# Performance work log

Hardware: AMD Instinct MI355X
Metric: run time of the kernel (lower is better)

## Reference

```python
import jax, jax.numpy as jnp
import numpy as np

N, E, F, C, H, O, ED = 100000, 1600000, 64, 64, 1, 32, 16
M = 20000  # number of masked (selected) nodes


def gat_layer(x, src, dst, edge_attr, W, a_s, a_d, We, a_e, b, n, h, c):
    # x: [n, in], W: [in, h*c], a_*: [h, c], We: [ed, h*c], b: [h*c]
    hx = (x @ W).reshape(n, h, c)                       # node features per head
    alpha_s = (hx * a_s).sum(-1)                        # [n, h]
    alpha_d = (hx * a_d).sum(-1)                        # [n, h]
    he = (edge_attr @ We).reshape(-1, h, c)             # [e, h, c]
    alpha = alpha_s[src] + alpha_d[dst] + (he * a_e).sum(-1)  # [e, h]
    alpha = jax.nn.leaky_relu(alpha, 0.2)
    # segment softmax over incoming edges of each destination node
    mx = jax.ops.segment_max(alpha, dst, num_segments=n)
    ex = jnp.exp(alpha - mx[dst])
    denom = jax.ops.segment_sum(ex, dst, num_segments=n)
    coef = ex / denom[dst]                              # [e, h]
    out = jax.ops.segment_sum(coef[:, :, None] * hx[src], dst, num_segments=n)
    return out.reshape(n, h * c) + b


def setup_inputs() -> dict:
    key = jax.random.key(0)
    ks = jax.random.split(key, 16)
    s = 0.1
    inp = {
        "x": jax.random.normal(ks[0], (N, F), jnp.float32),
        "edge_index": jax.random.randint(ks[1], (2, E), 0, N, jnp.int32),
        "mask": jax.random.randint(ks[2], (M,), 0, N, jnp.int32),
        "edge_attr": jax.random.normal(ks[3], (E, ED), jnp.float32),
        # conv1 params
        "W1": jax.random.normal(ks[4], (F, H * C), jnp.float32) * s,
        "a_s1": jax.random.normal(ks[5], (H, C), jnp.float32) * s,
        "a_d1": jax.random.normal(ks[6], (H, C), jnp.float32) * s,
        "We1": jax.random.normal(ks[7], (ED, H * C), jnp.float32) * s,
        "a_e1": jax.random.normal(ks[8], (H, C), jnp.float32) * s,
        "b1": jnp.zeros((H * C,), jnp.float32),
        # conv2 params
        "W2": jax.random.normal(ks[9], (H * C, H * O), jnp.float32) * s,
        "a_s2": jax.random.normal(ks[10], (H, O), jnp.float32) * s,
        "a_d2": jax.random.normal(ks[11], (H, O), jnp.float32) * s,
        "We2": jax.random.normal(ks[12], (ED, H * O), jnp.float32) * s,
        "a_e2": jax.random.normal(ks[13], (H, O), jnp.float32) * s,
        "b2": jnp.zeros((H * O,), jnp.float32),
    }
    return inp


def reference(x, edge_index, mask, edge_attr,
              W1, a_s1, a_d1, We1, a_e1, b1,
              W2, a_s2, a_d2, We2, a_e2, b2):
    # add self loops with fill_value=0 edge attributes (GATConv fill_value=0)
    loops = jnp.arange(N, dtype=edge_index.dtype)
    src = jnp.concatenate([edge_index[0], loops])
    dst = jnp.concatenate([edge_index[1], loops])
    ea = jnp.concatenate([edge_attr, jnp.zeros((N, ED), edge_attr.dtype)], axis=0)

    h1 = jax.nn.elu(gat_layer(x, src, dst, ea, W1, a_s1, a_d1, We1, a_e1, b1, N, H, C))
    h2 = jax.nn.elu(gat_layer(h1, src, dst, ea, W2, a_s2, a_d2, We2, a_e2, b2, N, H, O))
    return h2[mask]  # [M, O]; squeeze() is a no-op here
```

## Files before the change

### kernel.cpp

```cpp
#include <hip/hip_runtime.h>
#include <hip/hip_bf16.h>
#include <hip/hip_fp16.h>
#include <math.h>

#define NN 100000
#define EE 1600000
#define MM 20000
#define EPB 768
#define NBLK ((EE + EPB - 1) / EPB)
#define NBC 250
#define BWC 400
#define N_SCAN (NBC * NBLK + 1)
#define SMASK 0x1FFFF

__global__ void k_v(const float* __restrict__ We1, const float* __restrict__ ae1v,
                    const float* __restrict__ We2, const float* __restrict__ ae2v,
                    float* __restrict__ v1, float* __restrict__ v2) {
    int t = threadIdx.x;
    if (t < 16) {
        float s = 0.f;
        for (int c = 0; c < 64; ++c) s += We1[t * 64 + c] * ae1v[c];
        v1[t] = s;
    } else if (t < 32) {
        int r = t - 16;
        float s = 0.f;
        for (int c = 0; c < 32; ++c) s += We2[r * 32 + c] * ae2v[c];
        v2[r] = s;
    }
}

__global__ __launch_bounds__(256) void k_node1(
    const float* __restrict__ x, const float* __restrict__ W,
    const float* __restrict__ a_s, const float* __restrict__ a_d,
    __half* __restrict__ hx, float* __restrict__ aS, float* __restrict__ aD,
    int n_nodes)
{
    __shared__ float Wl[64 * 64];
    __shared__ float xs[4][64];
    int tid = threadIdx.x;
#pragma unroll
    for (int i = 0; i < 16; ++i) Wl[tid + i * 256] = W[tid + i * 256];
    int wv = tid >> 6, lane = tid & 63;
    int n = blockIdx.x * 4 + wv;
    bool act = (n < n_nodes);
    if (act) xs[wv][lane] = x[(size_t)n * 64 + lane];
    __syncthreads();
    if (!act) return;
    float h = 0.f;
#pragma unroll
    for (int k = 0; k < 64; ++k) h += xs[wv][k] * Wl[k * 64 + lane];
    hx[(size_t)n * 64 + lane] = __float2half(h);
    float ps = h * a_s[lane];
    float pd = h * a_d[lane];
#pragma unroll
    for (int o = 32; o > 0; o >>= 1) { ps += __shfl_xor(ps, o); pd += __shfl_xor(pd, o); }
    if (lane == 0) { aS[n] = ps; aD[n] = pd; }
}

__global__ __launch_bounds__(256) void k_bh(const int* __restrict__ dst,
                                            int* __restrict__ bh, int E) {
    __shared__ int hl[NBC];
    int tid = threadIdx.x, blk = blockIdx.x;
    for (int j = tid; j < NBC; j += 256) hl[j] = 0;
    __syncthreads();
    int e0 = blk * EPB, e1 = min(E, e0 + EPB);
    for (int e = e0 + tid; e < e1; e += 256) atomicAdd(&hl[dst[e] / BWC], 1);
    __syncthreads();
    for (int j = tid; j < NBC; j += 256) bh[j * NBLK + blk] = hl[j];
    if (blk == 0 && tid == 0) bh[NBC * NBLK] = 0;
}

__global__ __launch_bounds__(256) void k_scan1(const int* __restrict__ deg, int* __restrict__ pre,
                                               int* __restrict__ bsum, int n) {
    __shared__ int wsum[4];
    int t = threadIdx.x;
    int base = blockIdx.x * 2048 + t * 8;
    int v[8]; int s = 0;
#pragma unroll
    for (int i = 0; i < 8; ++i) { int idx = base + i; int d = (idx < n) ? deg[idx] : 0; v[i] = s; s += d; }
    int lane = t & 63, wv = t >> 6;
    int incl = s;
#pragma unroll
    for (int off = 1; off < 64; off <<= 1) { int y = __shfl_up(incl, off); if (lane >= off) incl += y; }
    if (lane == 63) wsum[wv] = incl;
    __syncthreads();
    int woff = 0;
    for (int w = 0; w < wv; ++w) woff += wsum[w];
    int texcl = woff + incl - s;
#pragma unroll
    for (int i = 0; i < 8; ++i) { int idx = base + i; if (idx < n) pre[idx] = texcl + v[i]; }
    if (t == 255) bsum[blockIdx.x] = woff + incl;
}

__global__ __launch_bounds__(256) void k_scan2(int* __restrict__ bsum, int nb) {
    __shared__ int ws[4];
    int t = threadIdx.x, lane = t & 63, wv = t >> 6;
    int x = (t < nb) ? bsum[t] : 0;
    int incl = x;
#pragma unroll
    for (int off = 1; off < 64; off <<= 1) { int y = __shfl_up(incl, off); if (lane >= off) incl += y; }
    if (lane == 63) ws[wv] = incl;
    __syncthreads();
    int woff = 0;
    for (int w = 0; w < wv; ++w) woff += ws[w];
    if (t < nb) bsum[t] = woff + incl - x;
}

__global__ void k_scan3b(int* __restrict__ pre, const int* __restrict__ bsum, int n) {
    int i = blockIdx.x * 256 + threadIdx.x;
    if (i < n) pre[i] += bsum[i >> 11];
}

__global__ __launch_bounds__(256) void k_part(
    const float* __restrict__ ea, const float* __restrict__ v1, const float* __restrict__ v2,
    const int* __restrict__ src, const int* __restrict__ dst,
    const float* __restrict__ aS1, const float* __restrict__ aD1,
    const int* __restrict__ scanned, uint2* __restrict__ recMid, int E)
{
    __shared__ int lcur[NBC];
    int tid = threadIdx.x, blk = blockIdx.x;
    for (int j = tid; j < NBC; j += 256) lcur[j] = scanned[j * NBLK + blk];
    __syncthreads();
    const float4* v14 = (const float4*)v1;
    const float4* v24 = (const float4*)v2;
    float4 va0 = v14[0], va1 = v14[1], va2 = v14[2], va3 = v14[3];
    float4 vb0 = v24[0], vb1 = v24[1], vb2 = v24[2], vb3 = v24[3];
    int e0 = blk * EPB, e1 = min(E, e0 + EPB);
    for (int e = e0 + tid; e < e1; e += 256) {
        const float4* p4 = (const float4*)(ea + (size_t)e * 16);
        float4 q0 = p4[0], q1 = p4[1], q2 = p4[2], q3 = p4[3];
        float s1 = q0.x * va0.x + q0.y * va0.y + q0.z * va0.z + q0.w * va0.w
                 + q1.x * va1.x + q1.y * va1.y + q1.z * va1.z + q1.w * va1.w
                 + q2.x * va2.x + q2.y * va2.y + q2.z * va2.z + q2.w * va2.w
                 + q3.x * va3.x + q3.y * va3.y + q3.z * va3.z + q3.w * va3.w;
        float s2 = q0.x * vb0.x + q0.y * vb0.y + q0.z * vb0.z + q0.w * vb0.w
                 + q1.x * vb1.x + q1.y * vb1.y + q1.z * vb1.z + q1.w * vb1.w
                 + q2.x * vb2.x + q2.y * vb2.y + q2.z * vb2.z + q2.w * vb2.w
                 + q3.x * vb3.x + q3.y * vb3.y + q3.z * vb3.z + q3.w * vb3.w;
        int s = src[e], d = dst[e];
        float a = aS1[s] + aD1[d] + s1;
        a = a > 0.f ? a : 0.2f * a;
        float ex = __expf(a);
        int b = d / BWC;
        int dloc = d - b * BWC;
        unsigned lo = (unsigned)s | ((unsigned)dloc << 17);
        unsigned hi = (unsigned)__half_as_ushort(__float2half(ex))
                    | ((unsigned)__half_as_ushort(__float2half(s2)) << 16);
        int pos = atomicAdd(&lcur[b], 1);
        recMid[pos] = make_uint2(lo, hi);
    }
}

__global__ __launch_bounds__(256) void k_build(
    const int* __restrict__ scanned, const uint2* __restrict__ recMid,
    int* __restrict__ rowptr, uint2* __restrict__ rec, int E)
{
    __shared__ int hist[BWC];
    __shared__ int lofs[BWC];
    __shared__ int wsum[4];
    int tid = threadIdx.x, b = blockIdx.x;
    int B0 = scanned[b * NBLK];
    int B1 = scanned[(b + 1) * NBLK];
    for (int j = tid; j < BWC; j += 256) hist[j] = 0;
    __syncthreads();
    for (int i = B0 + tid; i < B1; i += 256) atomicAdd(&hist[recMid[i].x >> 17], 1);
    __syncthreads();
    int lane = tid & 63, wv = tid >> 6;
    int i0 = 2 * tid, i1 = 2 * tid + 1;
    int a0 = (i0 < BWC) ? hist[i0] : 0;
    int a1 = (i1 < BWC) ? hist[i1] : 0;
    int s = a0 + a1;
    int incl = s;
#pragma unroll
    for (int off = 1; off < 64; off <<= 1) { int y = __shfl_up(incl, off); if (lane >= off) incl += y; }
    if (lane == 63) wsum[wv] = incl;
    __syncthreads();
    int woff = 0;
    for (int w = 0; w < wv; ++w) woff += wsum[w];
    int base = woff + incl - s;
    if (i0 < BWC) lofs[i0] = base;
    if (i1 < BWC) lofs[i1] = base + a0;
    __syncthreads();
    for (int j = tid; j < BWC; j += 256) rowptr[b * BWC + j] = B0 + lofs[j];
    if (b == NBC - 1 && tid == 0) rowptr[NN] = E;
    __syncthreads();
    for (int i = B0 + tid; i < B1; i += 256) {
        uint2 r = recMid[i];
        int nl = (int)(r.x >> 17);
        int p = atomicAdd(&lofs[nl], 1);
        rec[B0 + p] = r;
    }
}

__global__ __launch_bounds__(256) void k_agg1(
    const int* __restrict__ rowptr,
    const uint2* __restrict__ rec, const __half* __restrict__ hx,
    const float* __restrict__ aS, const float* __restrict__ aD,
    const float* __restrict__ b, float* __restrict__ h1, int n_nodes)
{
    int wv = threadIdx.x >> 6, lane = threadIdx.x & 63;
    int n = blockIdx.x * 4 + wv;
    if (n >= n_nodes) return;
    int start = rowptr[n], end = rowptr[n + 1];
    float r = 0.f, den = 0.f;
    for (int base = start; base < end; base += 64) {
        int cnt = min(end - base, 64);
        int s = 0; float ex = 0.f;
        if (lane < cnt) {
            uint2 R = rec[base + lane];
            s = (int)(R.x & SMASK);
            ex = __half2float(__ushort_as_half((unsigned short)(R.y & 0xFFFFu)));
        }
        int j = 0;
        for (; j + 4 <= cnt; j += 4) {
            int s0 = __shfl(s, j), s1 = __shfl(s, j + 1), s2 = __shfl(s, j + 2), s3 = __shfl(s, j + 3);
            float e0 = __shfl(ex, j), e1 = __shfl(ex, j + 1), e2 = __shfl(ex, j + 2), e3 = __shfl(ex, j + 3);
            float h0 = __half2float(hx[(size_t)s0 * 64 + lane]);
            float h1v = __half2float(hx[(size_t)s1 * 64 + lane]);
            float h2 = __half2float(hx[(size_t)s2 * 64 + lane]);
            float h3 = __half2float(hx[(size_t)s3 * 64 + lane]);
            r += e0 * h0; r += e1 * h1v; r += e2 * h2; r += e3 * h3;
            den += e0 + e1 + e2 + e3;
        }
        for (; j < cnt; ++j) {
            int sj = __shfl(s, j); float ej = __shfl(ex, j);
            r += ej * __half2float(hx[(size_t)sj * 64 + lane]);
            den += ej;
        }
    }
    float al = aS[n] + aD[n];
    al = al > 0.f ? al : 0.2f * al;
    float exl = __expf(al);
    float hself = __half2float(hx[(size_t)n * 64 + lane]);
    float val = (r + exl * hself) / (den + exl) + b[lane];
    h1[(size_t)n * 64 + lane] = val > 0.f ? val : expm1f(val);
}

__global__ __launch_bounds__(256) void k_node2(
    const float* __restrict__ h1, const float* __restrict__ W,
    const float* __restrict__ a_s, const float* __restrict__ a_d,
    float* __restrict__ hx, float* __restrict__ aS, float* __restrict__ aD, int n_nodes)
{
    __shared__ float Wl[64 * 32];
    __shared__ float xs[8][64];
    int tid = threadIdx.x;
#pragma unroll
    for (int i = 0; i < 8; ++i) Wl[tid + i * 256] = W[tid + i * 256];
    int n0 = blockIdx.x * 8;
    for (int i = tid; i < 8 * 64; i += 256) {
        int r = i >> 6;
        int n = n0 + r;
        xs[r][i & 63] = (n < n_nodes) ? h1[(size_t)n * 64 + (i & 63)] : 0.f;
    }
    __syncthreads();
    int g = tid >> 5, c = tid & 31;
    int n = n0 + g;
    if (n >= n_nodes) return;
    float h = 0.f;
#pragma unroll
    for (int k = 0; k < 64; ++k) h += xs[g][k] * Wl[k * 32 + c];
    hx[(size_t)n * 32 + c] = h;
    float ps = h * a_s[c], pd = h * a_d[c];
#pragma unroll
    for (int o = 16; o > 0; o >>= 1) { ps += __shfl_xor(ps, o, 32); pd += __shfl_xor(pd, o, 32); }
    if (c == 0) { aS[n] = ps; aD[n] = pd; }
}

__global__ __launch_bounds__(256) void k_agg2(
    const int* __restrict__ mask, const int* __restrict__ rowptr,
    const uint2* __restrict__ rec, const float* __restrict__ hx,
    const float* __restrict__ aS, const float* __restrict__ aD,
    const float* __restrict__ b, float* __restrict__ out, int m_cnt)
{
    int wv = threadIdx.x >> 6, lane = threadIdx.x & 63;
    int m = blockIdx.x * 4 + wv;
    if (m >= m_cnt) return;
    int n = mask[m];
    int start = rowptr[n], end = rowptr[n + 1];
    float aDn = aD[n];
    int half = lane >> 5, c = lane & 31;
    float r = 0.f, den = 0.f;
    for (int base = start; base < end; base += 64) {
        int cnt = min(end - base, 64);
        int s = 0; float ex = 0.f;
        if (lane < cnt) {
            uint2 R = rec[base + lane];
            s = (int)(R.x & SMASK);
            float ae2 = __half2float(__ushort_as_half((unsigned short)(R.y >> 16)));
            float a = aS[s] + aDn + ae2;
            a = a > 0.f ? a : 0.2f * a;
            ex = __expf(a);
        }
        int j = 0;
        for (; j + 8 <= cnt; j += 8) {
            int j0 = j + half, j2 = j + 2 + half, j4 = j + 4 + half, j6 = j + 6 + half;
            int s0 = __shfl(s, j0), s2v = __shfl(s, j2), s4 = __shfl(s, j4), s6 = __shfl(s, j6);
            float e0 = __shfl(ex, j0), e2 = __shfl(ex, j2), e4 = __shfl(ex, j4), e6 = __shfl(ex, j6);
            r += e0 * hx[(size_t)s0 * 32 + c];
            r += e2 * hx[(size_t)s2v * 32 + c];
            r += e4 * hx[(size_t)s4 * 32 + c];
            r += e6 * hx[(size_t)s6 * 32 + c];
            den += e0 + e2 + e4 + e6;
        }
        for (; j < cnt; j += 2) {
            int jj = j + half;
            if (jj < cnt) {
                int sj = __shfl(s, jj); float ej = __shfl(ex, jj);
                r += ej * hx[(size_t)sj * 32 + c];
                den += ej;
            }
        }
    }
    float ro = __shfl(r, lane ^ 32);
    float do_ = __shfl(den, lane ^ 32);
    r += ro; den += do_;
    if (half == 0) {
        float al = aS[n] + aDn;
        al = al > 0.f ? al : 0.2f * al;
        float exl = __expf(al);
        float val = (r + exl * hx[(size_t)n * 32 + c]) / (den + exl) + b[c];
        out[(size_t)m * 32 + c] = val > 0.f ? val : expm1f(val);
    }
}

extern "C" void kernel_launch(void* const* d_in, const int* in_sizes, int n_in,
                              void* d_out, int out_size, void* d_ws, size_t ws_size,
                              hipStream_t stream) {
    const float* x    = (const float*)d_in[0];
    const int*   ei   = (const int*)d_in[1];
    const int*   mask = (const int*)d_in[2];
    const float* ea   = (const float*)d_in[3];
    const float* W1   = (const float*)d_in[4];
    const float* a_s1 = (const float*)d_in[5];
    const float* a_d1 = (const float*)d_in[6];
    const float* We1  = (const float*)d_in[7];
    const float* a_e1 = (const float*)d_in[8];
    const float* b1   = (const float*)d_in[9];
    const float* W2   = (const float*)d_in[10];
    const float* a_s2 = (const float*)d_in[11];
    const float* a_d2 = (const float*)d_in[12];
    const float* We2  = (const float*)d_in[13];
    const float* a_e2 = (const float*)d_in[14];
    const float* b2   = (const float*)d_in[15];
    const int* src = ei;
    const int* dst = ei + EE;
    float* out = (float*)d_out;

    char* w = (char*)d_ws;
    size_t off = 0;
    auto take = [&](size_t bytes) -> char* {
        char* p = w + off;
        off += (bytes + 255) & ~(size_t)255;
        return p;
    };
    float*  v1      = (float*)take(16 * 4);
    float*  v2      = (float*)take(16 * 4);
    __half* hx1h    = (__half*)take((size_t)NN * 64 * 2);
    float*  aS1     = (float*)take((size_t)NN * 4);
    float*  aD1     = (float*)take((size_t)NN * 4);
    float*  h1      = (float*)take((size_t)NN * 64 * 4);
    float*  hx2     = (float*)take((size_t)NN * 32 * 4);
    float*  aS2     = (float*)take((size_t)NN * 4);
    float*  aD2     = (float*)take((size_t)NN * 4);
    int*    rowptr  = (int*)take(((size_t)NN + 1) * 4);
    int*    bh      = (int*)take((size_t)N_SCAN * 4);
    int*    scanned = (int*)take((size_t)N_SCAN * 4);
    int*    bsum    = (int*)take(256 * 4);
    uint2*  recMid  = (uint2*)take((size_t)EE * 8);
    uint2*  rec     = (uint2*)take((size_t)EE * 8);

    const int nb_bh = (N_SCAN + 2047) / 2048;

    k_v<<<1, 64, 0, stream>>>(We1, a_e1, We2, a_e2, v1, v2);
    k_node1<<<(NN + 3) / 4, 256, 0, stream>>>(x, W1, a_s1, a_d1, hx1h, aS1, aD1, NN);
    k_bh<<<NBLK, 256, 0, stream>>>(dst, bh, EE);
    k_scan1<<<nb_bh, 256, 0, stream>>>(bh, scanned, bsum, N_SCAN);
    k_scan2<<<1, 256, 0, stream>>>(bsum, nb_bh);
    k_scan3b<<<(N_SCAN + 255) / 256, 256, 0, stream>>>(scanned, bsum, N_SCAN);
    k_part<<<NBLK, 256, 0, stream>>>(ea, v1, v2, src, dst, aS1, aD1, scanned, recMid, EE);
    k_build<<<NBC, 256, 0, stream>>>(scanned, recMid, rowptr, rec, EE);
    k_agg1<<<(NN + 3) / 4, 256, 0, stream>>>(rowptr, rec, hx1h, aS1, aD1, b1, h1, NN);
    k_node2<<<(NN + 7) / 8, 256, 0, stream>>>(h1, W2, a_s2, a_d2, hx2, aS2, aD2, NN);
    k_agg2<<<(MM + 3) / 4, 256, 0, stream>>>(mask, rowptr, rec, hx2, aS2, aD2, b2, out, MM);
}
```

Before: 239.8 us.

## Move edge-attr projection into histogram pass and defer layer-1 exp to aggregation

```diff
diff --git a/kernel.cpp b/kernel.cpp
--- a/kernel.cpp
+++ b/kernel.cpp
@@ -57,69 +57,14 @@
     if (lane == 0) { aS[n] = ps; aD[n] = pd; }
 }
 
-__global__ __launch_bounds__(256) void k_bh(const int* __restrict__ dst,
-                                            int* __restrict__ bh, int E) {
+__global__ __launch_bounds__(256) void k_aebh(
+    const float* __restrict__ ea, const float* __restrict__ v1, const float* __restrict__ v2,
+    const int* __restrict__ dst, unsigned* __restrict__ ae12,
+    int* __restrict__ bh, int E)
+{
     __shared__ int hl[NBC];
     int tid = threadIdx.x, blk = blockIdx.x;
     for (int j = tid; j < NBC; j += 256) hl[j] = 0;
-    __syncthreads();
-    int e0 = blk * EPB, e1 = min(E, e0 + EPB);
-    for (int e = e0 + tid; e < e1; e += 256) atomicAdd(&hl[dst[e] / BWC], 1);
-    __syncthreads();
-    for (int j = tid; j < NBC; j += 256) bh[j * NBLK + blk] = hl[j];
-    if (blk == 0 && tid == 0) bh[NBC * NBLK] = 0;
-}
-
-__global__ __launch_bounds__(256) void k_scan1(const int* __restrict__ deg, int* __restrict__ pre,
-                                               int* __restrict__ bsum, int n) {
-    __shared__ int wsum[4];
-    int t = threadIdx.x;
-    int base = blockIdx.x * 2048 + t * 8;
-    int v[8]; int s = 0;
-#pragma unroll
-    for (int i = 0; i < 8; ++i) { int idx = base + i; int d = (idx < n) ? deg[idx] : 0; v[i] = s; s += d; }
-    int lane = t & 63, wv = t >> 6;
-    int incl = s;
-#pragma unroll
-    for (int off = 1; off < 64; off <<= 1) { int y = __shfl_up(incl, off); if (lane >= off) incl += y; }
-    if (lane == 63) wsum[wv] = incl;
-    __syncthreads();
-    int woff = 0;
-    for (int w = 0; w < wv; ++w) woff += wsum[w];
-    int texcl = woff + incl - s;
-#pragma unroll
-    for (int i = 0; i < 8; ++i) { int idx = base + i; if (idx < n) pre[idx] = texcl + v[i]; }
-    if (t == 255) bsum[blockIdx.x] = woff + incl;
-}
-
-__global__ __launch_bounds__(256) void k_scan2(int* __restrict__ bsum, int nb) {
-    __shared__ int ws[4];
-    int t = threadIdx.x, lane = t & 63, wv = t >> 6;
-    int x = (t < nb) ? bsum[t] : 0;
-    int incl = x;
-#pragma unroll
-    for (int off = 1; off < 64; off <<= 1) { int y = __shfl_up(incl, off); if (lane >= off) incl += y; }
-    if (lane == 63) ws[wv] = incl;
-    __syncthreads();
-    int woff = 0;
-    for (int w = 0; w < wv; ++w) woff += ws[w];
-    if (t < nb) bsum[t] = woff + incl - x;
-}
-
-__global__ void k_scan3b(int* __restrict__ pre, const int* __restrict__ bsum, int n) {
-    int i = blockIdx.x * 256 + threadIdx.x;
-    if (i < n) pre[i] += bsum[i >> 11];
-}
-
-__global__ __launch_bounds__(256) void k_part(
-    const float* __restrict__ ea, const float* __restrict__ v1, const float* __restrict__ v2,
-    const int* __restrict__ src, const int* __restrict__ dst,
-    const float* __restrict__ aS1, const float* __restrict__ aD1,
-    const int* __restrict__ scanned, uint2* __restrict__ recMid, int E)
-{
-    __shared__ int lcur[NBC];
-    int tid = threadIdx.x, blk = blockIdx.x;
-    for (int j = tid; j < NBC; j += 256) lcur[j] = scanned[j * NBLK + blk];
     __syncthreads();
     const float4* v14 = (const float4*)v1;
     const float4* v24 = (const float4*)v2;
@@ -137,17 +82,74 @@
                  + q1.x * vb1.x + q1.y * vb1.y + q1.z * vb1.z + q1.w * vb1.w
                  + q2.x * vb2.x + q2.y * vb2.y + q2.z * vb2.z + q2.w * vb2.w
                  + q3.x * vb3.x + q3.y * vb3.y + q3.z * vb3.z + q3.w * vb3.w;
+        ae12[e] = (unsigned)__half_as_ushort(__float2half(s1))
+                | ((unsigned)__half_as_ushort(__float2half(s2)) << 16);
+        atomicAdd(&hl[dst[e] / BWC], 1);
+    }
+    __syncthreads();
+    for (int j = tid; j < NBC; j += 256) bh[j * NBLK + blk] = hl[j];
+    if (blk == 0 && tid == 0) bh[NBC * NBLK] = 0;
+}
+
+__global__ __launch_bounds__(256) void k_scan1(const int* __restrict__ deg, int* __restrict__ pre,
+                                               int* __restrict__ bsum, int n) {
+    __shared__ int wsum[4];
+    int t = threadIdx.x;
+    int base = blockIdx.x * 2048 + t * 8;
+    int v[8]; int s = 0;
+#pragma unroll
+    for (int i = 0; i < 8; ++i) { int idx = base + i; int d = (idx < n) ? deg[idx] : 0; v[i] = s; s += d; }
+    int lane = t & 63, wv = t >> 6;
+    int incl = s;
+#pragma unroll
+    for (int off = 1; off < 64; off <<= 1) { int y = __shfl_up(incl, off); if (lane >= off) incl += y; }
+    if (lane == 63) wsum[wv] = incl;
+    __syncthreads();
+    int woff = 0;
+    for (int w = 0; w < wv; ++w) woff += wsum[w];
+    int texcl = woff + incl - s;
+#pragma unroll
+    for (int i = 0; i < 8; ++i) { int idx = base + i; if (idx < n) pre[idx] = texcl + v[i]; }
+    if (t == 255) bsum[blockIdx.x] = woff + incl;
+}
+
+__global__ __launch_bounds__(256) void k_scan2(int* __restrict__ bsum, int nb) {
+    __shared__ int ws[4];
+    int t = threadIdx.x, lane = t & 63, wv = t >> 6;
+    int x = (t < nb) ? bsum[t] : 0;
+    int incl = x;
+#pragma unroll
+    for (int off = 1; off < 64; off <<= 1) { int y = __shfl_up(incl, off); if (lane >= off) incl += y; }
+    if (lane == 63) ws[wv] = incl;
+    __syncthreads();
+    int woff = 0;
+    for (int w = 0; w < wv; ++w) woff += ws[w];
+    if (t < nb) bsum[t] = woff + incl - x;
+}
+
+__global__ void k_scan3b(int* __restrict__ pre, const int* __restrict__ bsum, int n) {
+    int i = blockIdx.x * 256 + threadIdx.x;
+    if (i < n) pre[i] += bsum[i >> 11];
+}
+
+__global__ __launch_bounds__(256) void k_part(
+    const int* __restrict__ src, const int* __restrict__ dst,
+    const unsigned* __restrict__ ae12,
+    const int* __restrict__ scanned, uint2* __restrict__ recMid, int E)
+{
+    __shared__ int lcur[NBC];
+    int tid = threadIdx.x, blk = blockIdx.x;
+    for (int j = tid; j < NBC; j += 256) lcur[j] = scanned[j * NBLK + blk];
+    __syncthreads();
+    int e0 = blk * EPB, e1 = min(E, e0 + EPB);
+    for (int e = e0 + tid; e < e1; e += 256) {
         int s = src[e], d = dst[e];
-        float a = aS1[s] + aD1[d] + s1;
-        a = a > 0.f ? a : 0.2f * a;
-        float ex = __expf(a);
+        unsigned w = ae12[e];
         int b = d / BWC;
         int dloc = d - b * BWC;
         unsigned lo = (unsigned)s | ((unsigned)dloc << 17);
-        unsigned hi = (unsigned)__half_as_ushort(__float2half(ex))
-                    | ((unsigned)__half_as_ushort(__float2half(s2)) << 16);
         int pos = atomicAdd(&lcur[b], 1);
-        recMid[pos] = make_uint2(lo, hi);
+        recMid[pos] = make_uint2(lo, w);
     }
 }
 
@@ -202,6 +204,7 @@
     int n = blockIdx.x * 4 + wv;
     if (n >= n_nodes) return;
     int start = rowptr[n], end = rowptr[n + 1];
+    float aDn = aD[n];
     float r = 0.f, den = 0.f;
     for (int base = start; base < end; base += 64) {
         int cnt = min(end - base, 64);
@@ -209,14 +212,17 @@
         if (lane < cnt) {
             uint2 R = rec[base + lane];
             s = (int)(R.x & SMASK);
-            ex = __half2float(__ushort_as_half((unsigned short)(R.y & 0xFFFFu)));
+            float s1 = __half2float(__ushort_as_half((unsigned short)(R.y & 0xFFFFu)));
+            float a = aS[s] + aDn + s1;
+            a = a > 0.f ? a : 0.2f * a;
+            ex = __expf(a);
         }
         int j = 0;
         for (; j + 4 <= cnt; j += 4) {
-            int s0 = __shfl(s, j), s1 = __shfl(s, j + 1), s2 = __shfl(s, j + 2), s3 = __shfl(s, j + 3);
+            int s0 = __shfl(s, j), s1i = __shfl(s, j + 1), s2 = __shfl(s, j + 2), s3 = __shfl(s, j + 3);
             float e0 = __shfl(ex, j), e1 = __shfl(ex, j + 1), e2 = __shfl(ex, j + 2), e3 = __shfl(ex, j + 3);
             float h0 = __half2float(hx[(size_t)s0 * 64 + lane]);
-            float h1v = __half2float(hx[(size_t)s1 * 64 + lane]);
+            float h1v = __half2float(hx[(size_t)s1i * 64 + lane]);
             float h2 = __half2float(hx[(size_t)s2 * 64 + lane]);
             float h3 = __half2float(hx[(size_t)s3 * 64 + lane]);
             r += e0 * h0; r += e1 * h1v; r += e2 * h2; r += e3 * h3;
@@ -228,7 +234,7 @@
             den += ej;
         }
     }
-    float al = aS[n] + aD[n];
+    float al = aS[n] + aDn;
     al = al > 0.f ? al : 0.2f * al;
     float exl = __expf(al);
     float hself = __half2float(hx[(size_t)n * 64 + lane]);
@@ -353,31 +359,32 @@
         off += (bytes + 255) & ~(size_t)255;
         return p;
     };
-    float*  v1      = (float*)take(16 * 4);
-    float*  v2      = (float*)take(16 * 4);
-    __half* hx1h    = (__half*)take((size_t)NN * 64 * 2);
-    float*  aS1     = (float*)take((size_t)NN * 4);
-    float*  aD1     = (float*)take((size_t)NN * 4);
-    float*  h1      = (float*)take((size_t)NN * 64 * 4);
-    float*  hx2     = (float*)take((size_t)NN * 32 * 4);
-    float*  aS2     = (float*)take((size_t)NN * 4);
-    float*  aD2     = (float*)take((size_t)NN * 4);
-    int*    rowptr  = (int*)take(((size_t)NN + 1) * 4);
-    int*    bh      = (int*)take((size_t)N_SCAN * 4);
-    int*    scanned = (int*)take((size_t)N_SCAN * 4);
-    int*    bsum    = (int*)take(256 * 4);
-    uint2*  recMid  = (uint2*)take((size_t)EE * 8);
-    uint2*  rec     = (uint2*)take((size_t)EE * 8);
+    float*    v1      = (float*)take(16 * 4);
+    float*    v2      = (float*)take(16 * 4);
+    __half*   hx1h    = (__half*)take((size_t)NN * 64 * 2);
+    float*    aS1     = (float*)take((size_t)NN * 4);
+    float*    aD1     = (float*)take((size_t)NN * 4);
+    float*    h1      = (float*)take((size_t)NN * 64 * 4);
+    float*    hx2     = (float*)take((size_t)NN * 32 * 4);
+    float*    aS2     = (float*)take((size_t)NN * 4);
+    float*    aD2     = (float*)take((size_t)NN * 4);
+    int*      rowptr  = (int*)take(((size_t)NN + 1) * 4);
+    unsigned* ae12    = (unsigned*)take((size_t)EE * 4);
+    int*      bh      = (int*)take((size_t)N_SCAN * 4);
+    int*      scanned = (int*)take((size_t)N_SCAN * 4);
+    int*      bsum    = (int*)take(256 * 4);
+    uint2*    recMid  = (uint2*)take((size_t)EE * 8);
+    uint2*    rec     = (uint2*)take((size_t)EE * 8);
 
     const int nb_bh = (N_SCAN + 2047) / 2048;
 
     k_v<<<1, 64, 0, stream>>>(We1, a_e1, We2, a_e2, v1, v2);
     k_node1<<<(NN + 3) / 4, 256, 0, stream>>>(x, W1, a_s1, a_d1, hx1h, aS1, aD1, NN);
-    k_bh<<<NBLK, 256, 0, stream>>>(dst, bh, EE);
+    k_aebh<<<NBLK, 256, 0, stream>>>(ea, v1, v2, dst, ae12, bh, EE);
     k_scan1<<<nb_bh, 256, 0, stream>>>(bh, scanned, bsum, N_SCAN);
     k_scan2<<<1, 256, 0, stream>>>(bsum, nb_bh);
     k_scan3b<<<(N_SCAN + 255) / 256, 256, 0, stream>>>(scanned, bsum, N_SCAN);
-    k_part<<<NBLK, 256, 0, stream>>>(ea, v1, v2, src, dst, aS1, aD1, scanned, recMid, EE);
+    k_part<<<NBLK, 256, 0, stream>>>(src, dst, ae12, scanned, recMid, EE);
     k_build<<<NBC, 256, 0, stream>>>(scanned, recMid, rowptr, rec, EE);
     k_agg1<<<(NN + 3) / 4, 256, 0, stream>>>(rowptr, rec, hx1h, aS1, aD1, b1, h1, NN);
     k_node2<<<(NN + 7) / 8, 256, 0, stream>>>(h1, W2, a_s2, a_d2, hx2, aS2, aD2, NN);
```

Result: no change. 240.3 us (+0.2%).
